# Performance work log

Hardware: AMD Instinct MI355X
Metric: run time of the kernel (lower is better)

The kernel has to match this reference:

```python
import jax, jax.numpy as jnp
import numpy as np

BS, NF, NT = 64, 18, 1500
HID = 256
LH = HID // 2          # lstm hidden dim = 128
T, NC = 6, 2           # 6 detector layers, 2 coords per layer
POS_FEATS = HID // 4   # 64


def lstm_layer(x_seq, W_ih, W_hh, b_ih, b_hh):
    """x_seq: [T, B, D] -> (all hidden states [T, B, H], final hidden [B, H]).
    PyTorch gate order: input, forget, cell(g), output."""
    B = x_seq.shape[1]
    H = W_hh.shape[1]
    h0 = jnp.zeros((B, H), x_seq.dtype)

    def step(carry, x_t):
        h, c = carry
        gates = x_t @ W_ih.T + h @ W_hh.T + (b_ih + b_hh)
        i, f, g, o = jnp.split(gates, 4, axis=-1)
        c = jax.nn.sigmoid(f) * c + jax.nn.sigmoid(i) * jnp.tanh(g)
        h = jax.nn.sigmoid(o) * jnp.tanh(c)
        return (h, c), h

    (hT, _), hs = jax.lax.scan(step, (h0, h0), x_seq)
    return hs, hT


def build_pos_embed_from_eta_phi(deta, dphi, num_feats):
    """DETR-style sine/cosine embedding; output [..., 2*num_feats]."""
    scale = 2.0 * np.pi
    temperature = 10000.0
    dim_t = temperature ** (2.0 * (jnp.arange(num_feats) // 2).astype(jnp.float32) / num_feats)

    def enc(x):
        p = x[..., None] * scale / dim_t                        # [..., num_feats]
        out = jnp.stack([jnp.sin(p[..., 0::2]), jnp.cos(p[..., 1::2])], axis=-1)
        return out.reshape(*p.shape[:-1], num_feats)

    return jnp.concatenate([enc(deta), enc(dphi)], axis=-1)


def setup_inputs() -> dict:
    key = jax.random.key(0)
    ks = jax.random.split(key, 16)
    s = 0.05
    inp = {
        "track_feats": jax.random.normal(ks[0], (BS, NF, NT), dtype=jnp.float32),
        # LSTM layer 0 (input size 2)
        "W_ih0": jax.random.normal(ks[1], (4 * LH, NC), dtype=jnp.float32) * s,
        "W_hh0": jax.random.normal(ks[2], (4 * LH, LH), dtype=jnp.float32) * s,
        "b_ih0": jax.random.normal(ks[3], (4 * LH,), dtype=jnp.float32) * s,
        "b_hh0": jax.random.normal(ks[4], (4 * LH,), dtype=jnp.float32) * s,
        # LSTM layer 1 (input size LH)
        "W_ih1": jax.random.normal(ks[5], (4 * LH, LH), dtype=jnp.float32) * s,
        "W_hh1": jax.random.normal(ks[6], (4 * LH, LH), dtype=jnp.float32) * s,
        "b_ih1": jax.random.normal(ks[7], (4 * LH,), dtype=jnp.float32) * s,
        "b_hh1": jax.random.normal(ks[8], (4 * LH,), dtype=jnp.float32) * s,
        # MLP: (3 + LH) -> HID -> HID, ReLU between
        "mlp_w0": jax.random.normal(ks[9], (HID, 3 + LH), dtype=jnp.float32) * s,
        "mlp_b0": jnp.zeros((HID,), dtype=jnp.float32),
        "mlp_w1": jax.random.normal(ks[10], (HID, HID), dtype=jnp.float32) * s,
        "mlp_b1": jnp.zeros((HID,), dtype=jnp.float32),
    }
    return inp


def reference(track_feats, W_ih0, W_hh0, b_ih0, b_hh0, W_ih1, W_hh1, b_ih1, b_hh1,
              mlp_w0, mlp_b0, mlp_w1, mlp_b1):
    tf = jnp.transpose(track_feats, (0, 2, 1))      # [bs, n_track, 18]
    bs, n_track, _ = tf.shape
    eta = tf[..., 3]
    phi = tf[..., 4]
    logpt = tf[..., 2]

    traj = tf[..., 6:6 + T * NC].reshape(bs * n_track, T, NC)
    x_seq = jnp.transpose(traj, (1, 0, 2))           # [T, bs*n_track, 2]
    hs0, _ = lstm_layer(x_seq, W_ih0, W_hh0, b_ih0, b_hh0)
    _, hT1 = lstm_layer(hs0, W_ih1, W_hh1, b_ih1, b_hh1)
    traj_emb = hT1.reshape(bs, n_track, LH)

    combined = jnp.concatenate([tf[..., 0:3], traj_emb], axis=-1)  # [bs, nt, 3+LH]
    h = jax.nn.relu(combined @ mlp_w0.T + mlp_b0)
    final_embedding = h @ mlp_w1.T + mlp_b1          # [bs, nt, HID]

    pos_encoding = build_pos_embed_from_eta_phi(eta, phi, POS_FEATS)  # [bs, nt, HID//2]
    return (final_embedding, pos_encoding, logpt, eta, phi)
```

## Files before the change

kernel.cpp:

```cpp
#include <hip/hip_runtime.h>
#include <math.h>

#define NTRK   1500
#define BSZ    64
#define NTOT   (NTRK*BSZ)
#define LHID   128
#define TSTEPS 6
#define HID    256

#define TPB    256
#define TPBM   512
#define MTRK   64
#define NBLK   (NTOT/MTRK)

#define WHH0_OFF 0
#define WIH1_OFF 65536
#define WHH1_OFF 131072
#define W0B_OFF  196608
#define W1B_OFF  229376
#define BX_OFF   294912
#define WS_SHORTS 299008

#define OUT1_OFF ((size_t)NTOT*HID)
#define OUT2_OFF (OUT1_OFF + (size_t)NTOT*(HID/2))
#define OUT3_OFF (OUT2_OFF + (size_t)NTOT)
#define OUT4_OFF (OUT3_OFF + (size_t)NTOT)

typedef __bf16 bf16x8 __attribute__((ext_vector_type(8)));
typedef float  f32x4  __attribute__((ext_vector_type(4)));

__device__ __forceinline__ unsigned short f2b(float f) {
    union { float f; unsigned u; } v; v.f = f;
    return (unsigned short)((v.u + 0x7FFF + ((v.u >> 16) & 1)) >> 16);
}
__device__ __forceinline__ float sigf(float x) { return 1.0f / (1.0f + __expf(-x)); }
__device__ __forceinline__ float tanhfast(float x) {
    float e = __expf(2.0f * x);
    return (e - 1.0f) / (e + 1.0f);
}

__global__ __launch_bounds__(TPB)
void prep_kernel(const float* __restrict__ Whh0, const float* __restrict__ Wih1,
                 const float* __restrict__ Whh1, const float* __restrict__ w0,
                 const float* __restrict__ w1,  const float* __restrict__ Wih0,
                 const float* __restrict__ bih0, const float* __restrict__ bhh0,
                 unsigned short* __restrict__ ws)
{
    int i = blockIdx.x * TPB + threadIdx.x;
    if (i < 65536)            ws[WHH0_OFF + i] = f2b(Whh0[i]);
    else if (i < 131072)      ws[WIH1_OFF + (i - 65536)]  = f2b(Wih1[i - 65536]);
    else if (i < 196608)      ws[WHH1_OFF + (i - 131072)] = f2b(Whh1[i - 131072]);
    else if (i < 229376) { int j = i - 196608; int n = j >> 7, k = j & 127;
                           ws[W0B_OFF + j] = f2b(w0[n * 131 + 3 + k]); }
    else if (i < 294912)      ws[W1B_OFF + (i - 229376)]  = f2b(w1[i - 229376]);
    else if (i < WS_SHORTS) { int j = i - 294912; int n = j >> 3, k = j & 7;
                              float v = (k == 0) ? Wih0[2 * n]
                                      : (k == 1) ? Wih0[2 * n + 1]
                                      : (k == 2) ? (bih0[n] + bhh0[n]) : 0.0f;
                              ws[BX_OFF + j] = f2b(v); }
}

__device__ __forceinline__ int aoff4(int m, int k) {
    return (((m >> 4) * 4 + (k >> 5)) * 64 + ((k >> 3) & 3) * 16 + (m & 15)) * 8 + (k & 7);
}
__device__ __forceinline__ int aoff8(int m, int k) {
    return (((m >> 4) * 8 + (k >> 5)) * 64 + ((k >> 3) & 3) * 16 + (m & 15)) * 8 + (k & 7);
}

template<int TI>
__device__ __forceinline__ void accum4(f32x4 (&acc)[4][TI],
                                       const unsigned short* __restrict__ Wb,
                                       const unsigned short* hA,
                                       const int (&rowb)[TI], int lane, int quad)
{
    #pragma unroll
    for (int kk = 0; kk < 4; ++kk) {
        bf16x8 a[4];
        #pragma unroll
        for (int mt = 0; mt < 4; ++mt)
            a[mt] = *(const bf16x8*)&hA[((mt * 4 + kk) * 64 + lane) * 8];
        #pragma unroll
        for (int ti = 0; ti < TI; ++ti) {
            bf16x8 b = *(const bf16x8*)&Wb[(size_t)rowb[ti] * 128 + kk * 32 + quad * 8];
            #pragma unroll
            for (int mt = 0; mt < 4; ++mt)
                acc[mt][ti] = __builtin_amdgcn_mfma_f32_16x16x32_bf16(a[mt], b, acc[mt][ti], 0, 0, 0);
        }
    }
}

__global__ __launch_bounds__(TPBM, 4)
void lstm_mlp_mfma(const float* __restrict__ tfeat,
                   const float* __restrict__ bih1, const float* __restrict__ bhh1,
                   const float* __restrict__ w0,  const float* __restrict__ b0,
                   const float* __restrict__ b1,
                   const unsigned short* __restrict__ wsb,
                   float* __restrict__ out)
{
    __shared__ __align__(16) char smem[68096];
    unsigned short* hA0_0 = (unsigned short*)smem;
    unsigned short* hA0_1 = (unsigned short*)(smem + 16384);
    unsigned short* hA1_0 = (unsigned short*)(smem + 32768);
    unsigned short* hA1_1 = (unsigned short*)(smem + 49152);
    unsigned short* mhA   = (unsigned short*)smem;
    unsigned short* xbh   = (unsigned short*)(smem + 65536);
    float (*f3)[4]  = (float(*)[4])(smem + 67072);
    float* outb = (float*)smem;

    const int tid  = threadIdx.x;
    const int w    = tid >> 6;
    const int lane = tid & 63;
    const int col  = lane & 15;
    const int quad = lane >> 4;
    const int base = blockIdx.x * MTRK;

    for (int idx = tid; idx < MTRK * 12; idx += TPBM) {
        int tl = idx & 63, f = idx >> 6;
        int n = base + tl, b = n / NTRK, tt = n - b * NTRK;
        xbh[tl * 12 + f] = f2b(tfeat[(size_t)(b * 18 + 6 + f) * NTRK + tt]);
    }
    for (int idx = tid; idx < MTRK * 3; idx += TPBM) {
        int tl = idx & 63, f = idx >> 6;
        int n = base + tl, b = n / NTRK, tt = n - b * NTRK;
        f3[tl][f] = tfeat[(size_t)(b * 18 + f) * NTRK + tt];
    }
    __syncthreads();

    const unsigned short* Whh0b = wsb + WHH0_OFF;
    const unsigned short* Wih1b = wsb + WIH1_OFF;
    const unsigned short* Whh1b = wsb + WHH1_OFF;
    const unsigned short* w0b   = wsb + W0B_OFF;
    const unsigned short* w1b   = wsb + W1B_OFF;
    const unsigned short* Bx    = wsb + BX_OFF;

    int   rowg[4];
    float bs1[4];
    #pragma unroll
    for (int g = 0; g < 4; ++g) {
        int n = g * 128 + w * 16 + col;
        rowg[g] = n;
        bs1[g] = bih1[n] + bhh1[n];
    }

    f32x4 c0[4], c1[4];
    #pragma unroll
    for (int mt = 0; mt < 4; ++mt)
        #pragma unroll
        for (int r = 0; r < 4; ++r) { c0[mt][r] = 0.0f; c1[mt][r] = 0.0f; }

    const int u = w * 16 + col;

    for (int t = 0; t < TSTEPS; ++t) {
        const int cur = t & 1;
        unsigned short* h0c       = cur ? hA0_1 : hA0_0;
        const unsigned short* h0p = cur ? hA0_0 : hA0_1;
        unsigned short* h1c       = cur ? hA1_1 : hA1_0;
        const unsigned short* h1p = cur ? hA1_0 : hA1_1;

        f32x4 acc[4][4];
        {
            bf16x8 ax[4];
            #pragma unroll
            for (int mt = 0; mt < 4; ++mt) {
                bf16x8 a;
                #pragma unroll
                for (int j = 0; j < 8; ++j) a[j] = (__bf16)0.0f;
                if (quad == 0) {
                    int m = mt * 16 + col;
                    a[0] = *(const __bf16*)&xbh[m * 12 + 2 * t];
                    a[1] = *(const __bf16*)&xbh[m * 12 + 2 * t + 1];
                    a[2] = (__bf16)1.0f;
                }
                ax[mt] = a;
            }
            #pragma unroll
            for (int g = 0; g < 4; ++g) {
                bf16x8 bx;
                #pragma unroll
                for (int j = 0; j < 8; ++j) bx[j] = (__bf16)0.0f;
                if (quad == 0) bx = *(const bf16x8*)&Bx[rowg[g] * 8];
                #pragma unroll
                for (int mt = 0; mt < 4; ++mt) {
                    f32x4 z = {0.0f, 0.0f, 0.0f, 0.0f};
                    acc[mt][g] = __builtin_amdgcn_mfma_f32_16x16x32_bf16(ax[mt], bx, z, 0, 0, 0);
                }
            }
        }
        if (t > 0) accum4<4>(acc, Whh0b, h0p, rowg, lane, quad);
        #pragma unroll
        for (int mt = 0; mt < 4; ++mt)
            #pragma unroll
            for (int r = 0; r < 4; ++r) {
                float iv = sigf(acc[mt][0][r]);
                float fv = sigf(acc[mt][1][r]);
                float gv = tanhfast(acc[mt][2][r]);
                float ov = sigf(acc[mt][3][r]);
                float cn = fv * c0[mt][r] + iv * gv;
                c0[mt][r] = cn;
                int m = mt * 16 + quad * 4 + r;
                h0c[aoff4(m, u)] = f2b(ov * tanhfast(cn));
            }
        __syncthreads();

        #pragma unroll
        for (int mt = 0; mt < 4; ++mt)
            #pragma unroll
            for (int g = 0; g < 4; ++g)
                #pragma unroll
                for (int r = 0; r < 4; ++r) acc[mt][g][r] = bs1[g];
        accum4<4>(acc, Wih1b, h0c, rowg, lane, quad);
        if (t > 0) accum4<4>(acc, Whh1b, h1p, rowg, lane, quad);
        #pragma unroll
        for (int mt = 0; mt < 4; ++mt)
            #pragma unroll
            for (int r = 0; r < 4; ++r) {
                float iv = sigf(acc[mt][0][r]);
                float fv = sigf(acc[mt][1][r]);
                float gv = tanhfast(acc[mt][2][r]);
                float ov = sigf(acc[mt][3][r]);
                float cn = fv * c1[mt][r] + iv * gv;
                c1[mt][r] = cn;
                int m = mt * 16 + quad * 4 + r;
                h1c[aoff4(m, u)] = f2b(ov * tanhfast(cn));
            }
        __syncthreads();
    }

    const unsigned short* h1f = hA1_1;

    int rowm[2];
    #pragma unroll
    for (int ti = 0; ti < 2; ++ti) rowm[ti] = w * 32 + ti * 16 + col;

    {
        f32x4 am[4][2];
        #pragma unroll
        for (int ti = 0; ti < 2; ++ti) {
            int n = rowm[ti];
            float bm  = b0[n];
            float wf0 = w0[n * 131 + 0], wf1 = w0[n * 131 + 1], wf2 = w0[n * 131 + 2];
            #pragma unroll
            for (int mt = 0; mt < 4; ++mt)
                #pragma unroll
                for (int r = 0; r < 4; ++r) {
                    int m = mt * 16 + quad * 4 + r;
                    am[mt][ti][r] = bm + f3[m][0] * wf0 + f3[m][1] * wf1 + f3[m][2] * wf2;
                }
        }
        accum4<2>(am, w0b, h1f, rowm, lane, quad);
        #pragma unroll
        for (int mt = 0; mt < 4; ++mt)
            #pragma unroll
            for (int ti = 0; ti < 2; ++ti)
                #pragma unroll
                for (int r = 0; r < 4; ++r) {
                    int m = mt * 16 + quad * 4 + r;
                    mhA[aoff8(m, w * 32 + ti * 16 + col)] = f2b(fmaxf(am[mt][ti][r], 0.0f));
                }
        __syncthreads();
    }

    {
        f32x4 ao[4][2];
        #pragma unroll
        for (int ti = 0; ti < 2; ++ti) {
            float bv = b1[rowm[ti]];
            #pragma unroll
            for (int mt = 0; mt < 4; ++mt)
                #pragma unroll
                for (int r = 0; r < 4; ++r) ao[mt][ti][r] = bv;
        }
        #pragma unroll
        for (int kk = 0; kk < 8; ++kk) {
            bf16x8 a[4];
            #pragma unroll
            for (int mt = 0; mt < 4; ++mt)
                a[mt] = *(const bf16x8*)&mhA[((mt * 8 + kk) * 64 + lane) * 8];
            #pragma unroll
            for (int ti = 0; ti < 2; ++ti) {
                bf16x8 b = *(const bf16x8*)&w1b[(size_t)rowm[ti] * 256 + kk * 32 + quad * 8];
                #pragma unroll
                for (int mt = 0; mt < 4; ++mt)
                    ao[mt][ti] = __builtin_amdgcn_mfma_f32_16x16x32_bf16(a[mt], b, ao[mt][ti], 0, 0, 0);
            }
        }
        __syncthreads();

        #pragma unroll
        for (int mt = 0; mt < 4; ++mt)
            #pragma unroll
            for (int ti = 0; ti < 2; ++ti)
                #pragma unroll
                for (int r = 0; r < 4; ++r)
                    outb[(mt * 16 + quad * 4 + r) * 260 + w * 32 + ti * 16 + col] = ao[mt][ti][r];
        __syncthreads();

        for (int i = tid; i < MTRK * 64; i += TPBM) {
            int row = i >> 6, c4 = (i & 63) << 2;
            f32x4 v = *(const f32x4*)&outb[row * 260 + c4];
            __builtin_nontemporal_store(v, (f32x4*)(out + (size_t)(base + row) * HID + c4));
        }
    }
}

__global__ __launch_bounds__(TPB)
void pos_kernel(const float* __restrict__ tfeat, float* __restrict__ out)
{
    const int idx = blockIdx.x * TPB + threadIdx.x;
    const int m = idx & 31;
    const int n = idx >> 5;
    const int b = n / NTRK, tt = n - b * NTRK;

    const float eta = tfeat[(size_t)(b * 18 + 3) * NTRK + tt];
    const float phi = tfeat[(size_t)(b * 18 + 4) * NTRK + tt];

    const float inv = exp2f(-(float)m * (13.28771237954945f / 32.0f));
    const float TWO_PI = 6.28318530717958647692f;
    const float pe = eta * TWO_PI * inv;
    const float pp = phi * TWO_PI * inv;

    float* o1 = out + OUT1_OFF + (size_t)n * (HID / 2);
    __builtin_nontemporal_store(sinf(pe), o1 + 2 * m);
    __builtin_nontemporal_store(cosf(pe), o1 + 2 * m + 1);
    __builtin_nontemporal_store(sinf(pp), o1 + 64 + 2 * m);
    __builtin_nontemporal_store(cosf(pp), o1 + 64 + 2 * m + 1);

    if (m == 0) {
        __builtin_nontemporal_store(tfeat[(size_t)(b * 18 + 2) * NTRK + tt], out + OUT2_OFF + n);
        __builtin_nontemporal_store(eta, out + OUT3_OFF + n);
        __builtin_nontemporal_store(phi, out + OUT4_OFF + n);
    }
}

extern "C" void kernel_launch(void* const* d_in, const int* in_sizes, int n_in,
                              void* d_out, int out_size, void* d_ws, size_t ws_size,
                              hipStream_t stream)
{
    const float* tfeat = (const float*)d_in[0];
    const float* Wih0  = (const float*)d_in[1];
    const float* Whh0  = (const float*)d_in[2];
    const float* bih0  = (const float*)d_in[3];
    const float* bhh0  = (const float*)d_in[4];
    const float* Wih1  = (const float*)d_in[5];
    const float* Whh1  = (const float*)d_in[6];
    const float* bih1  = (const float*)d_in[7];
    const float* bhh1  = (const float*)d_in[8];
    const float* w0    = (const float*)d_in[9];
    const float* b0    = (const float*)d_in[10];
    const float* w1    = (const float*)d_in[11];
    const float* b1    = (const float*)d_in[12];
    float* out = (float*)d_out;
    unsigned short* wsb = (unsigned short*)d_ws;

    hipLaunchKernelGGL(prep_kernel, dim3(WS_SHORTS / TPB), dim3(TPB), 0, stream,
                       Whh0, Wih1, Whh1, w0, w1, Wih0, bih0, bhh0, wsb);
    hipLaunchKernelGGL(lstm_mlp_mfma, dim3(NBLK), dim3(TPBM), 0, stream,
                       tfeat, bih1, bhh1, w0, b0, b1, wsb, out);
    hipLaunchKernelGGL(pos_kernel, dim3((NTOT * 32) / TPB), dim3(TPB), 0, stream,
                       tfeat, out);
}
```

Baseline: 1.069 ms.

## Split LSTM gate accumulation into pairs and fuse positional encoding into main kernel

Each LSTM step now computes the gates in two passes: first input and cell gates, which are combined into one product, then forget and output gates. This halves the live accumulator registers, aiming at less register pressure or spilling under the 4-blocks-per-CU launch bound. The separate positional-encoding kernel is removed. Its sin/cos embedding and pass-through outputs are now computed at the end of the main kernel from eta/phi staged in shared memory, which drops a launch and a second read of the features. In exchange, the x-input MFMA setup is recomputed for each gate pair, and the sin/cos work is added to the tail of the heavy kernel.

```diff
diff --git a/kernel.cpp b/kernel.cpp
--- a/kernel.cpp
+++ b/kernel.cpp
@@ -28,6 +28,7 @@
 
 typedef __bf16 bf16x8 __attribute__((ext_vector_type(8)));
 typedef float  f32x4  __attribute__((ext_vector_type(4)));
+typedef float  f32x2  __attribute__((ext_vector_type(2)));
 
 __device__ __forceinline__ unsigned short f2b(float f) {
     union { float f; unsigned u; } v; v.f = f;
@@ -67,11 +68,10 @@
     return (((m >> 4) * 8 + (k >> 5)) * 64 + ((k >> 3) & 3) * 16 + (m & 15)) * 8 + (k & 7);
 }
 
-template<int TI>
-__device__ __forceinline__ void accum4(f32x4 (&acc)[4][TI],
-                                       const unsigned short* __restrict__ Wb,
-                                       const unsigned short* hA,
-                                       const int (&rowb)[TI], int lane, int quad)
+__device__ __forceinline__ void accum2t(f32x4 (&acc)[4][2],
+                                        const unsigned short* __restrict__ Wb,
+                                        const unsigned short* hA,
+                                        const int (&rowb)[2], int lane, int quad)
 {
     #pragma unroll
     for (int kk = 0; kk < 4; ++kk) {
@@ -80,7 +80,7 @@
         for (int mt = 0; mt < 4; ++mt)
             a[mt] = *(const bf16x8*)&hA[((mt * 4 + kk) * 64 + lane) * 8];
         #pragma unroll
-        for (int ti = 0; ti < TI; ++ti) {
+        for (int ti = 0; ti < 2; ++ti) {
             bf16x8 b = *(const bf16x8*)&Wb[(size_t)rowb[ti] * 128 + kk * 32 + quad * 8];
             #pragma unroll
             for (int mt = 0; mt < 4; ++mt)
@@ -97,14 +97,14 @@
                    const unsigned short* __restrict__ wsb,
                    float* __restrict__ out)
 {
-    __shared__ __align__(16) char smem[68096];
+    __shared__ __align__(16) char smem[69120];
     unsigned short* hA0_0 = (unsigned short*)smem;
     unsigned short* hA0_1 = (unsigned short*)(smem + 16384);
     unsigned short* hA1_0 = (unsigned short*)(smem + 32768);
     unsigned short* hA1_1 = (unsigned short*)(smem + 49152);
     unsigned short* mhA   = (unsigned short*)smem;
     unsigned short* xbh   = (unsigned short*)(smem + 65536);
-    float (*f3)[4]  = (float(*)[4])(smem + 67072);
+    float (*f5)[8]  = (float(*)[8])(smem + 67072);
     float* outb = (float*)smem;
 
     const int tid  = threadIdx.x;
@@ -119,10 +119,10 @@
         int n = base + tl, b = n / NTRK, tt = n - b * NTRK;
         xbh[tl * 12 + f] = f2b(tfeat[(size_t)(b * 18 + 6 + f) * NTRK + tt]);
     }
-    for (int idx = tid; idx < MTRK * 3; idx += TPBM) {
-        int tl = idx & 63, f = idx >> 6;
+    if (tid < MTRK * 5) {
+        int tl = tid & 63, f = tid >> 6;
         int n = base + tl, b = n / NTRK, tt = n - b * NTRK;
-        f3[tl][f] = tfeat[(size_t)(b * 18 + f) * NTRK + tt];
+        f5[tl][f] = tfeat[(size_t)(b * 18 + f) * NTRK + tt];
     }
     __syncthreads();
 
@@ -141,6 +141,8 @@
         rowg[g] = n;
         bs1[g] = bih1[n] + bhh1[n];
     }
+    const int rows_ig[2] = { rowg[0], rowg[2] };
+    const int rows_fo[2] = { rowg[1], rowg[3] };
 
     f32x4 c0[4], c1[4];
     #pragma unroll
@@ -157,72 +159,126 @@
         unsigned short* h1c       = cur ? hA1_1 : hA1_0;
         const unsigned short* h1p = cur ? hA1_0 : hA1_1;
 
-        f32x4 acc[4][4];
+        f32x4 p0[4];
         {
-            bf16x8 ax[4];
-            #pragma unroll
-            for (int mt = 0; mt < 4; ++mt) {
-                bf16x8 a;
-                #pragma unroll
-                for (int j = 0; j < 8; ++j) a[j] = (__bf16)0.0f;
-                if (quad == 0) {
-                    int m = mt * 16 + col;
-                    a[0] = *(const __bf16*)&xbh[m * 12 + 2 * t];
-                    a[1] = *(const __bf16*)&xbh[m * 12 + 2 * t + 1];
-                    a[2] = (__bf16)1.0f;
-                }
-                ax[mt] = a;
+            f32x4 acc[4][2];
+            {
+                bf16x8 ax[4];
+                #pragma unroll
+                for (int mt = 0; mt < 4; ++mt) {
+                    bf16x8 a;
+                    #pragma unroll
+                    for (int j = 0; j < 8; ++j) a[j] = (__bf16)0.0f;
+                    if (quad == 0) {
+                        int m = mt * 16 + col;
+                        a[0] = *(const __bf16*)&xbh[m * 12 + 2 * t];
+                        a[1] = *(const __bf16*)&xbh[m * 12 + 2 * t + 1];
+                        a[2] = (__bf16)1.0f;
+                    }
+                    ax[mt] = a;
+                }
+                #pragma unroll
+                for (int ti = 0; ti < 2; ++ti) {
+                    bf16x8 bx;
+                    #pragma unroll
+                    for (int j = 0; j < 8; ++j) bx[j] = (__bf16)0.0f;
+                    if (quad == 0) bx = *(const bf16x8*)&Bx[rows_ig[ti] * 8];
+                    #pragma unroll
+                    for (int mt = 0; mt < 4; ++mt) {
+                        f32x4 z = {0.0f, 0.0f, 0.0f, 0.0f};
+                        acc[mt][ti] = __builtin_amdgcn_mfma_f32_16x16x32_bf16(ax[mt], bx, z, 0, 0, 0);
+                    }
+                }
             }
-            #pragma unroll
-            for (int g = 0; g < 4; ++g) {
-                bf16x8 bx;
-                #pragma unroll
-                for (int j = 0; j < 8; ++j) bx[j] = (__bf16)0.0f;
-                if (quad == 0) bx = *(const bf16x8*)&Bx[rowg[g] * 8];
+            if (t > 0) accum2t(acc, Whh0b, h0p, rows_ig, lane, quad);
+            #pragma unroll
+            for (int mt = 0; mt < 4; ++mt)
+                #pragma unroll
+                for (int r = 0; r < 4; ++r)
+                    p0[mt][r] = sigf(acc[mt][0][r]) * tanhfast(acc[mt][1][r]);
+        }
+        {
+            f32x4 acc[4][2];
+            {
+                bf16x8 ax[4];
                 #pragma unroll
                 for (int mt = 0; mt < 4; ++mt) {
-                    f32x4 z = {0.0f, 0.0f, 0.0f, 0.0f};
-                    acc[mt][g] = __builtin_amdgcn_mfma_f32_16x16x32_bf16(ax[mt], bx, z, 0, 0, 0);
+                    bf16x8 a;
+                    #pragma unroll
+                    for (int j = 0; j < 8; ++j) a[j] = (__bf16)0.0f;
+                    if (quad == 0) {
+                        int m = mt * 16 + col;
+                        a[0] = *(const __bf16*)&xbh[m * 12 + 2 * t];
+                        a[1] = *(const __bf16*)&xbh[m * 12 + 2 * t + 1];
+                        a[2] = (__bf16)1.0f;
+                    }
+                    ax[mt] = a;
+                }
+                #pragma unroll
+                for (int ti = 0; ti < 2; ++ti) {
+                    bf16x8 bx;
+                    #pragma unroll
+                    for (int j = 0; j < 8; ++j) bx[j] = (__bf16)0.0f;
+                    if (quad == 0) bx = *(const bf16x8*)&Bx[rows_fo[ti] * 8];
+                    #pragma unroll
+                    for (int mt = 0; mt < 4; ++mt) {
+                        f32x4 z = {0.0f, 0.0f, 0.0f, 0.0f};
+                        acc[mt][ti] = __builtin_amdgcn_mfma_f32_16x16x32_bf16(ax[mt], bx, z, 0, 0, 0);
+                    }
                 }
             }
-        }
-        if (t > 0) accum4<4>(acc, Whh0b, h0p, rowg, lane, quad);
-        #pragma unroll
-        for (int mt = 0; mt < 4; ++mt)
-            #pragma unroll
-            for (int r = 0; r < 4; ++r) {
-                float iv = sigf(acc[mt][0][r]);
-                float fv = sigf(acc[mt][1][r]);
-                float gv = tanhfast(acc[mt][2][r]);
-                float ov = sigf(acc[mt][3][r]);
-                float cn = fv * c0[mt][r] + iv * gv;
-                c0[mt][r] = cn;
-                int m = mt * 16 + quad * 4 + r;
-                h0c[aoff4(m, u)] = f2b(ov * tanhfast(cn));
-            }
+            if (t > 0) accum2t(acc, Whh0b, h0p, rows_fo, lane, quad);
+            #pragma unroll
+            for (int mt = 0; mt < 4; ++mt)
+                #pragma unroll
+                for (int r = 0; r < 4; ++r) {
+                    float cn = sigf(acc[mt][0][r]) * c0[mt][r] + p0[mt][r];
+                    c0[mt][r] = cn;
+                    int m = mt * 16 + quad * 4 + r;
+                    h0c[aoff4(m, u)] = f2b(sigf(acc[mt][1][r]) * tanhfast(cn));
+                }
+        }
         __syncthreads();
 
-        #pragma unroll
-        for (int mt = 0; mt < 4; ++mt)
-            #pragma unroll
-            for (int g = 0; g < 4; ++g)
-                #pragma unroll
-                for (int r = 0; r < 4; ++r) acc[mt][g][r] = bs1[g];
-        accum4<4>(acc, Wih1b, h0c, rowg, lane, quad);
-        if (t > 0) accum4<4>(acc, Whh1b, h1p, rowg, lane, quad);
-        #pragma unroll
-        for (int mt = 0; mt < 4; ++mt)
-            #pragma unroll
-            for (int r = 0; r < 4; ++r) {
-                float iv = sigf(acc[mt][0][r]);
-                float fv = sigf(acc[mt][1][r]);
-                float gv = tanhfast(acc[mt][2][r]);
-                float ov = sigf(acc[mt][3][r]);
-                float cn = fv * c1[mt][r] + iv * gv;
-                c1[mt][r] = cn;
-                int m = mt * 16 + quad * 4 + r;
-                h1c[aoff4(m, u)] = f2b(ov * tanhfast(cn));
-            }
+        f32x4 p1[4];
+        {
+            f32x4 acc[4][2];
+            #pragma unroll
+            for (int mt = 0; mt < 4; ++mt)
+                #pragma unroll
+                for (int r = 0; r < 4; ++r) {
+                    acc[mt][0][r] = bs1[0];
+                    acc[mt][1][r] = bs1[2];
+                }
+            accum2t(acc, Wih1b, h0c, rows_ig, lane, quad);
+            if (t > 0) accum2t(acc, Whh1b, h1p, rows_ig, lane, quad);
+            #pragma unroll
+            for (int mt = 0; mt < 4; ++mt)
+                #pragma unroll
+                for (int r = 0; r < 4; ++r)
+                    p1[mt][r] = sigf(acc[mt][0][r]) * tanhfast(acc[mt][1][r]);
+        }
+        {
+            f32x4 acc[4][2];
+            #pragma unroll
+            for (int mt = 0; mt < 4; ++mt)
+                #pragma unroll
+                for (int r = 0; r < 4; ++r) {
+                    acc[mt][0][r] = bs1[1];
+                    acc[mt][1][r] = bs1[3];
+                }
+            accum2t(acc, Wih1b, h0c, rows_fo, lane, quad);
+            if (t > 0) accum2t(acc, Whh1b, h1p, rows_fo, lane, quad);
+            #pragma unroll
+            for (int mt = 0; mt < 4; ++mt)
+                #pragma unroll
+                for (int r = 0; r < 4; ++r) {
+                    float cn = sigf(acc[mt][0][r]) * c1[mt][r] + p1[mt][r];
+                    c1[mt][r] = cn;
+                    int m = mt * 16 + quad * 4 + r;
+                    h1c[aoff4(m, u)] = f2b(sigf(acc[mt][1][r]) * tanhfast(cn));
+                }
+        }
         __syncthreads();
     }
 
@@ -244,10 +300,10 @@
                 #pragma unroll
                 for (int r = 0; r < 4; ++r) {
                     int m = mt * 16 + quad * 4 + r;
-                    am[mt][ti][r] = bm + f3[m][0] * wf0 + f3[m][1] * wf1 + f3[m][2] * wf2;
-                }
-        }
-        accum4<2>(am, w0b, h1f, rowm, lane, quad);
+                    am[mt][ti][r] = bm + f5[m][0] * wf0 + f5[m][1] * wf1 + f5[m][2] * wf2;
+                }
+        }
+        accum2t(am, w0b, h1f, rowm, lane, quad);
         #pragma unroll
         for (int mt = 0; mt < 4; ++mt)
             #pragma unroll
@@ -301,34 +357,31 @@
             __builtin_nontemporal_store(v, (f32x4*)(out + (size_t)(base + row) * HID + c4));
         }
     }
-}
-
-__global__ __launch_bounds__(TPB)
-void pos_kernel(const float* __restrict__ tfeat, float* __restrict__ out)
-{
-    const int idx = blockIdx.x * TPB + threadIdx.x;
-    const int m = idx & 31;
-    const int n = idx >> 5;
-    const int b = n / NTRK, tt = n - b * NTRK;
-
-    const float eta = tfeat[(size_t)(b * 18 + 3) * NTRK + tt];
-    const float phi = tfeat[(size_t)(b * 18 + 4) * NTRK + tt];
-
-    const float inv = exp2f(-(float)m * (13.28771237954945f / 32.0f));
-    const float TWO_PI = 6.28318530717958647692f;
-    const float pe = eta * TWO_PI * inv;
-    const float pp = phi * TWO_PI * inv;
-
-    float* o1 = out + OUT1_OFF + (size_t)n * (HID / 2);
-    __builtin_nontemporal_store(sinf(pe), o1 + 2 * m);
-    __builtin_nontemporal_store(cosf(pe), o1 + 2 * m + 1);
-    __builtin_nontemporal_store(sinf(pp), o1 + 64 + 2 * m);
-    __builtin_nontemporal_store(cosf(pp), o1 + 64 + 2 * m + 1);
-
-    if (m == 0) {
-        __builtin_nontemporal_store(tfeat[(size_t)(b * 18 + 2) * NTRK + tt], out + OUT2_OFF + n);
-        __builtin_nontemporal_store(eta, out + OUT3_OFF + n);
-        __builtin_nontemporal_store(phi, out + OUT4_OFF + n);
+
+    {
+        const int tl = tid >> 3;
+        const int ml = tid & 7;
+        const int n  = base + tl;
+        const float eta   = f5[tl][3];
+        const float phi   = f5[tl][4];
+        const float TWO_PI = 6.28318530717958647692f;
+        float* o1 = out + OUT1_OFF + (size_t)n * (HID / 2);
+        #pragma unroll
+        for (int i = 0; i < 4; ++i) {
+            int m = ml + i * 8;
+            float inv = exp2f(-(float)m * (13.28771237954945f / 32.0f));
+            float pe = eta * TWO_PI * inv;
+            float pp = phi * TWO_PI * inv;
+            f32x2 ve = { sinf(pe), cosf(pe) };
+            f32x2 vp = { sinf(pp), cosf(pp) };
+            __builtin_nontemporal_store(ve, (f32x2*)(o1 + 2 * m));
+            __builtin_nontemporal_store(vp, (f32x2*)(o1 + 64 + 2 * m));
+        }
+        if (ml == 0) {
+            __builtin_nontemporal_store(f5[tl][2], out + OUT2_OFF + n);
+            __builtin_nontemporal_store(eta, out + OUT3_OFF + n);
+            __builtin_nontemporal_store(phi, out + OUT4_OFF + n);
+        }
     }
 }
 
@@ -356,6 +409,4 @@
                        Whh0, Wih1, Whh1, w0, w1, Wih0, bih0, bhh0, wsb);
     hipLaunchKernelGGL(lstm_mlp_mfma, dim3(NBLK), dim3(TPBM), 0, stream,
                        tfeat, bih1, bhh1, w0, b0, b1, wsb, out);
-    hipLaunchKernelGGL(pos_kernel, dim3((NTOT * 32) / TPB), dim3(TPB), 0, stream,
-                       tfeat, out);
-}
+}
```

After: 1.123 ms. 5.0% more time.

## Fuse positional-encoding kernel into LSTM/MLP kernel epilogue

Applied to the files above, without the earlier changes.

Removes the separate pos_kernel launch and computes the sine/cosine positional embedding plus the logpt/eta/phi copies at the end of the LSTM/MLP kernel. The eta/phi/logpt values are reused from a shared-memory staging array that now holds 5 features instead of 3, and stores are paired into float2. The launch bound's minimum blocks per CU drops from 4 to 2, which loosens the register cap and may change occupancy. This saves a launch and a reread of tfeat, but adds transcendental work to the tail of the main kernel.

```diff
diff --git a/kernel.cpp b/kernel.cpp
--- a/kernel.cpp
+++ b/kernel.cpp
@@ -28,6 +28,7 @@
 
 typedef __bf16 bf16x8 __attribute__((ext_vector_type(8)));
 typedef float  f32x4  __attribute__((ext_vector_type(4)));
+typedef float  f32x2  __attribute__((ext_vector_type(2)));
 
 __device__ __forceinline__ unsigned short f2b(float f) {
     union { float f; unsigned u; } v; v.f = f;
@@ -89,7 +90,7 @@
     }
 }
 
-__global__ __launch_bounds__(TPBM, 4)
+__global__ __launch_bounds__(TPBM, 2)
 void lstm_mlp_mfma(const float* __restrict__ tfeat,
                    const float* __restrict__ bih1, const float* __restrict__ bhh1,
                    const float* __restrict__ w0,  const float* __restrict__ b0,
@@ -97,14 +98,14 @@
                    const unsigned short* __restrict__ wsb,
                    float* __restrict__ out)
 {
-    __shared__ __align__(16) char smem[68096];
+    __shared__ __align__(16) char smem[69120];
     unsigned short* hA0_0 = (unsigned short*)smem;
     unsigned short* hA0_1 = (unsigned short*)(smem + 16384);
     unsigned short* hA1_0 = (unsigned short*)(smem + 32768);
     unsigned short* hA1_1 = (unsigned short*)(smem + 49152);
     unsigned short* mhA   = (unsigned short*)smem;
     unsigned short* xbh   = (unsigned short*)(smem + 65536);
-    float (*f3)[4]  = (float(*)[4])(smem + 67072);
+    float (*f5)[8]  = (float(*)[8])(smem + 67072);
     float* outb = (float*)smem;
 
     const int tid  = threadIdx.x;
@@ -119,10 +120,10 @@
         int n = base + tl, b = n / NTRK, tt = n - b * NTRK;
         xbh[tl * 12 + f] = f2b(tfeat[(size_t)(b * 18 + 6 + f) * NTRK + tt]);
     }
-    for (int idx = tid; idx < MTRK * 3; idx += TPBM) {
-        int tl = idx & 63, f = idx >> 6;
+    if (tid < MTRK * 5) {
+        int tl = tid & 63, f = tid >> 6;
         int n = base + tl, b = n / NTRK, tt = n - b * NTRK;
-        f3[tl][f] = tfeat[(size_t)(b * 18 + f) * NTRK + tt];
+        f5[tl][f] = tfeat[(size_t)(b * 18 + f) * NTRK + tt];
     }
     __syncthreads();
 
@@ -244,7 +245,7 @@
                 #pragma unroll
                 for (int r = 0; r < 4; ++r) {
                     int m = mt * 16 + quad * 4 + r;
-                    am[mt][ti][r] = bm + f3[m][0] * wf0 + f3[m][1] * wf1 + f3[m][2] * wf2;
+                    am[mt][ti][r] = bm + f5[m][0] * wf0 + f5[m][1] * wf1 + f5[m][2] * wf2;
                 }
         }
         accum4<2>(am, w0b, h1f, rowm, lane, quad);
@@ -301,34 +302,31 @@
             __builtin_nontemporal_store(v, (f32x4*)(out + (size_t)(base + row) * HID + c4));
         }
     }
-}
-
-__global__ __launch_bounds__(TPB)
-void pos_kernel(const float* __restrict__ tfeat, float* __restrict__ out)
-{
-    const int idx = blockIdx.x * TPB + threadIdx.x;
-    const int m = idx & 31;
-    const int n = idx >> 5;
-    const int b = n / NTRK, tt = n - b * NTRK;
-
-    const float eta = tfeat[(size_t)(b * 18 + 3) * NTRK + tt];
-    const float phi = tfeat[(size_t)(b * 18 + 4) * NTRK + tt];
-
-    const float inv = exp2f(-(float)m * (13.28771237954945f / 32.0f));
-    const float TWO_PI = 6.28318530717958647692f;
-    const float pe = eta * TWO_PI * inv;
-    const float pp = phi * TWO_PI * inv;
-
-    float* o1 = out + OUT1_OFF + (size_t)n * (HID / 2);
-    __builtin_nontemporal_store(sinf(pe), o1 + 2 * m);
-    __builtin_nontemporal_store(cosf(pe), o1 + 2 * m + 1);
-    __builtin_nontemporal_store(sinf(pp), o1 + 64 + 2 * m);
-    __builtin_nontemporal_store(cosf(pp), o1 + 64 + 2 * m + 1);
-
-    if (m == 0) {
-        __builtin_nontemporal_store(tfeat[(size_t)(b * 18 + 2) * NTRK + tt], out + OUT2_OFF + n);
-        __builtin_nontemporal_store(eta, out + OUT3_OFF + n);
-        __builtin_nontemporal_store(phi, out + OUT4_OFF + n);
+
+    {
+        const int tl = tid >> 3;
+        const int ml = tid & 7;
+        const int n  = base + tl;
+        const float eta   = f5[tl][3];
+        const float phi   = f5[tl][4];
+        const float TWO_PI = 6.28318530717958647692f;
+        float* o1 = out + OUT1_OFF + (size_t)n * (HID / 2);
+        #pragma unroll
+        for (int i = 0; i < 4; ++i) {
+            int m = ml + i * 8;
+            float inv = exp2f(-(float)m * (13.28771237954945f / 32.0f));
+            float pe = eta * TWO_PI * inv;
+            float pp = phi * TWO_PI * inv;
+            f32x2 ve = { sinf(pe), cosf(pe) };
+            f32x2 vp = { sinf(pp), cosf(pp) };
+            __builtin_nontemporal_store(ve, (f32x2*)(o1 + 2 * m));
+            __builtin_nontemporal_store(vp, (f32x2*)(o1 + 64 + 2 * m));
+        }
+        if (ml == 0) {
+            __builtin_nontemporal_store(f5[tl][2], out + OUT2_OFF + n);
+            __builtin_nontemporal_store(eta, out + OUT3_OFF + n);
+            __builtin_nontemporal_store(phi, out + OUT4_OFF + n);
+        }
     }
 }
 
@@ -356,6 +354,4 @@
                        Whh0, Wih1, Whh1, w0, w1, Wih0, bih0, bhh0, wsb);
     hipLaunchKernelGGL(lstm_mlp_mfma, dim3(NBLK), dim3(TPBM), 0, stream,
                        tfeat, bih1, bhh1, w0, b0, b1, wsb, out);
-    hipLaunchKernelGGL(pos_kernel, dim3((NTOT * 32) / TPB), dim3(TPB), 0, stream,
-                       tfeat, out);
-}
+}
```

New measurement: 876.6 us. 1.22x faster.
